# Optimization experiments

Measured on AMD Instinct MI355X. Metric: run time of the kernel, lower is better.

Reference implementation:

```python
import jax, jax.numpy as jnp
import numpy as np

B, N, DIN, D, PHI, RHO, L = 4096, 10, 32, 128, 256, 128, 3
EPS = 1e-5


def setup_inputs() -> dict:
    key = jax.random.key(0)
    ks = jax.random.split(key, 24)
    def p(k, shape):
        return jax.random.normal(k, shape, jnp.float32) * 0.05
    return {
        "A": jax.random.normal(ks[0], (B, N, N), jnp.float32),
        "X": jax.random.normal(ks[1], (B, N, DIN), jnp.float32),
        "home_mask": jax.random.randint(ks[2], (B, N), 0, 2).astype(jnp.int32),
        "We1": p(ks[3], (DIN, D)), "be1": p(ks[4], (D,)),
        "We2": p(ks[5], (D, D)), "be2": p(ks[6], (D,)),
        "rgcn_w": p(ks[7], (L, 2, D, D)),      # per-relation weights
        "rgcn_root": p(ks[8], (L, D, D)),       # root (self) weight
        "rgcn_b": p(ks[9], (L, D)),
        "l1w": p(ks[10], (L, D, D)), "l1b": p(ks[11], (L, D)),
        "l2w": p(ks[12], (L, D, D)), "l2b": p(ks[13], (L, D)),
        "ln_g": jnp.ones((D,), jnp.float32), "ln_b": jnp.zeros((D,), jnp.float32),
        "p1w": p(ks[14], (D, PHI)), "p1b": p(ks[15], (PHI,)),
        "p2w": p(ks[16], (PHI, PHI)), "p2b": p(ks[17], (PHI,)),
        "r1w": p(ks[18], (PHI, RHO)), "r1b": p(ks[19], (RHO,)),
        "r2w": p(ks[20], (RHO, 1)), "r2b": p(ks[21], (1,)),
    }


def _layernorm(x, g, b):
    mu = x.mean(-1, keepdims=True)
    var = ((x - mu) ** 2).mean(-1, keepdims=True)
    return (x - mu) / jnp.sqrt(var + EPS) * g + b


def reference(A, X, home_mask, We1, be1, We2, be2, rgcn_w, rgcn_root, rgcn_b,
              l1w, l1b, l2w, l2b, ln_g, ln_b, p1w, p1b, p2w, p2b,
              r1w, r1b, r2w, r2b):
    BN = B * N
    hm = home_mask.astype(jnp.float32)
    am = 1.0 - hm
    # embedders (dropout layers are identity in eval)
    H = jax.nn.relu(X @ We1 + be1)
    H = (H @ We2 + be2).reshape(BN, D)
    # A ~ randn is nonzero everywhere -> edge list = all (b,i,j) pairs,
    # in the same row-major order torch.nonzero produces.
    bidx = jnp.repeat(jnp.arange(BN), N)          # b*N+i for each edge (row)
    row = bidx
    col = (jnp.repeat(jnp.arange(B), N * N) * N + jnp.tile(jnp.arange(N), BN))
    ew = A.reshape(-1)                             # edge weight
    aw = jnp.abs(ew)
    m1 = (ew > 0).astype(jnp.float32)              # relation 1 mask
    m0 = 1.0 - m1                                  # relation 0 mask
    agg = jnp.zeros_like(H)
    for l in range(L):
        H = H + agg
        # RGCNConv (mean aggregation per relation + root + bias)
        xj = H[row]                                # [E, D] gather of sources
        s0 = jax.ops.segment_sum(xj * m0[:, None], col, num_segments=BN)
        s1 = jax.ops.segment_sum(xj * m1[:, None], col, num_segments=BN)
        c0 = jax.ops.segment_sum(m0, col, num_segments=BN)
        c1 = jax.ops.segment_sum(m1, col, num_segments=BN)
        mean0 = s0 / jnp.maximum(c0, 1.0)[:, None]
        mean1 = s1 / jnp.maximum(c1, 1.0)[:, None]
        H2 = mean0 @ rgcn_w[l, 0] + mean1 @ rgcn_w[l, 1] + H @ rgcn_root[l] + rgcn_b[l]
        # outer gather-scale-scatter
        msg = H2[col] * aw[:, None]                # [E, D]
        agg = jax.ops.segment_sum(msg, row, num_segments=BN)
        agg = jax.nn.relu(_layernorm(agg, ln_g, ln_b))
        # Linear -> ReLU -> (Dropout=id) -> Linear
        agg = jax.nn.relu(agg @ l1w[l] + l1b[l])
        agg = agg @ l2w[l] + l2b[l]
    H = (H + agg).reshape(B, N, D)
    # DeepSet phi (dropout = identity)
    phi = jax.nn.relu(H @ p1w + p1b)
    phi = jax.nn.relu(phi @ p2w + p2b)             # [B, N, PHI]
    hs = (phi * hm[..., None]).sum(axis=1)
    aws = (phi * am[..., None]).sum(axis=1)
    def rho(s):
        return (jax.nn.relu(s @ r1w + r1b) @ r2w + r2b)[..., 0]
    return 0.5 + 0.5 * jnp.tanh(rho(hs) - rho(aws))
```

## Files before the change

### kernel.cpp

```cpp
#include <hip/hip_runtime.h>
#include <math.h>

#define B_    4096
#define N_    10
#define DIN_  32
#define D_    128
#define PHI_  256
#define RHO_  128
#define L_    3
#define EPS_  1e-5f

__device__ __forceinline__ short f2bs(float f) {
    unsigned u = __float_as_uint(f);
    u += 0x7fffu + ((u >> 16) & 1u);
    return (short)(u >> 16);
}
__device__ __forceinline__ float bs2f(short s) {
    return __uint_as_float(((unsigned)(unsigned short)s) << 16);
}

typedef short bf16x8 __attribute__((ext_vector_type(8)));
typedef float f32x4  __attribute__((ext_vector_type(4)));
typedef float v2f    __attribute__((ext_vector_type(2)));

__device__ __forceinline__ v2f splat2(float s) { v2f r; r.x = s; r.y = s; return r; }
__device__ __forceinline__ v2f fma2(v2f a, v2f b, v2f c) { return __builtin_elementwise_fma(a, b, c); }

#define WS_WE1 0
#define WS_WE2 4096
#define WS_RGW 20480
#define WS_RGR 118784
#define WS_L1  167936
#define WS_L2  217088
#define WS_P1  266240
#define WS_P2  299008
#define WS_R1  364544

__global__ __launch_bounds__(64)
void prep_weights(const float* __restrict__ We1, const float* __restrict__ We2,
                  const float* __restrict__ rgw, const float* __restrict__ rgr,
                  const float* __restrict__ l1w, const float* __restrict__ l2w,
                  const float* __restrict__ p1w, const float* __restrict__ p2w,
                  const float* __restrict__ r1w, short* __restrict__ ws)
{
    int bi = blockIdx.x, l = threadIdx.x;
    const float* src; int KS, Nw, dstOff, tt;
    if      (bi <   8) { src = We1; KS = 1; Nw = 128; dstOff = WS_WE1; tt = bi; }
    else if (bi <  40) { src = We2; KS = 4; Nw = 128; dstOff = WS_WE2; tt = bi - 8; }
    else if (bi < 232) { int m = (bi - 40) >> 5;  src = rgw + m * 16384; KS = 4; Nw = 128; dstOff = WS_RGW + m * 16384; tt = (bi - 40)  & 31; }
    else if (bi < 328) { int m = (bi - 232) >> 5; src = rgr + m * 16384; KS = 4; Nw = 128; dstOff = WS_RGR + m * 16384; tt = (bi - 232) & 31; }
    else if (bi < 424) { int m = (bi - 328) >> 5; src = l1w + m * 16384; KS = 4; Nw = 128; dstOff = WS_L1  + m * 16384; tt = (bi - 328) & 31; }
    else if (bi < 520) { int m = (bi - 424) >> 5; src = l2w + m * 16384; KS = 4; Nw = 128; dstOff = WS_L2  + m * 16384; tt = (bi - 424) & 31; }
    else if (bi < 584) { src = p1w; KS = 4; Nw = 256; dstOff = WS_P1; tt = bi - 520; }
    else if (bi < 712) { src = p2w; KS = 8; Nw = 256; dstOff = WS_P2; tt = bi - 584; }
    else               { src = r1w; KS = 8; Nw = 128; dstOff = WS_R1; tt = bi - 712; }
    int nt = tt / KS, ks = tt - nt * KS;
    int kbase = ks * 32 + (l >> 4) * 8;
    int col   = nt * 16 + (l & 15);
    union { short s[8]; int4 v; } u;
#pragma unroll
    for (int j = 0; j < 8; ++j)
        u.s[j] = f2bs(src[(size_t)(kbase + j) * Nw + col]);
    *(int4*)(ws + dstOff + ((size_t)tt * 64 + l) * 8) = u.v;
}


template<int NT>
__device__ __forceinline__ void initC(f32x4* acc, const float* __restrict__ bias, int c16) {
#pragma unroll
    for (int nt = 0; nt < NT; ++nt) {
        float bv = bias[nt * 16 + c16];
        acc[nt] = (f32x4){bv, bv, bv, bv};
    }
}

template<int KS, int NT>
__device__ __forceinline__ void mm_a16(const short* __restrict__ Wf, const short* __restrict__ Ab,
                                       int ldA, int mrow, int q, int l, f32x4* acc) {
#pragma unroll
    for (int ks = 0; ks < KS; ++ks) {
        bf16x8 a = *(const bf16x8*)(Ab + mrow * ldA + ks * 32 + q * 8);
#pragma unroll
        for (int nt = 0; nt < NT; ++nt) {
            bf16x8 bv = *(const bf16x8*)(Wf + ((size_t)(nt * KS + ks) * 64 + l) * 8);
            acc[nt] = __builtin_amdgcn_mfma_f32_16x16x32_bf16(a, bv, acc[nt], 0, 0, 0);
        }
    }
}

template<int KS, int NT>
__device__ __forceinline__ void mm_a32(const short* __restrict__ Wf, const float* __restrict__ Af,
                                       int ldA, int mrow, int q, int l, f32x4* acc) {
#pragma unroll
    for (int ks = 0; ks < KS; ++ks) {
        const float* p = Af + mrow * ldA + ks * 32 + q * 8;
        f32x4 x0 = *(const f32x4*)p;
        f32x4 x1 = *(const f32x4*)(p + 4);
        bf16x8 a;
        a[0] = f2bs(x0[0]); a[1] = f2bs(x0[1]); a[2] = f2bs(x0[2]); a[3] = f2bs(x0[3]);
        a[4] = f2bs(x1[0]); a[5] = f2bs(x1[1]); a[6] = f2bs(x1[2]); a[7] = f2bs(x1[3]);
#pragma unroll
        for (int nt = 0; nt < NT; ++nt) {
            bf16x8 bv = *(const bf16x8*)(Wf + ((size_t)(nt * KS + ks) * 64 + l) * 8);
            acc[nt] = __builtin_amdgcn_mfma_f32_16x16x32_bf16(a, bv, acc[nt], 0, 0, 0);
        }
    }
}

template<int KS>
__device__ __forceinline__ void mm8p_a16(const short* __restrict__ Wf,
                                         const short* __restrict__ Ab, int ldA,
                                         int mrow, int q, int l, f32x4* acc)
{
    const short* ap = Ab + mrow * ldA + q * 8;
    const short* wp = Wf + l * 8;
    bf16x8 acur = *(const bf16x8*)ap;
    bf16x8 bcur[8], bnxt[8];
#pragma unroll
    for (int nt = 0; nt < 8; ++nt) bcur[nt] = *(const bf16x8*)(wp + (size_t)nt * KS * 512);
#pragma unroll
    for (int ks = 0; ks < KS; ++ks) {
        bf16x8 anxt = acur;
#pragma unroll
        for (int nt = 0; nt < 8; ++nt) bnxt[nt] = bcur[nt];
        if (ks + 1 < KS) {
            anxt = *(const bf16x8*)(ap + (ks + 1) * 32);
#pragma unroll
            for (int nt = 0; nt < 8; ++nt)
                bnxt[nt] = *(const bf16x8*)(wp + (size_t)(nt * KS + ks + 1) * 512);
        }
#pragma unroll
        for (int nt = 0; nt < 8; ++nt)
            acc[nt] = __builtin_amdgcn_mfma_f32_16x16x32_bf16(acur, bcur[nt], acc[nt], 0, 0, 0);
        acur = anxt;
#pragma unroll
        for (int nt = 0; nt < 8; ++nt) bcur[nt] = bnxt[nt];
    }
}

template<int KS>
__device__ __forceinline__ void mm8p_a32(const short* __restrict__ Wf,
                                         const float* __restrict__ Af, int ldA,
                                         int mrow, int q, int l, f32x4* acc)
{
    const float* ap = Af + mrow * ldA + q * 8;
    const short* wp = Wf + l * 8;
    auto cvt = [&](int ks) {
        f32x4 x0 = *(const f32x4*)(ap + ks * 32);
        f32x4 x1 = *(const f32x4*)(ap + ks * 32 + 4);
        bf16x8 a;
        a[0] = f2bs(x0[0]); a[1] = f2bs(x0[1]); a[2] = f2bs(x0[2]); a[3] = f2bs(x0[3]);
        a[4] = f2bs(x1[0]); a[5] = f2bs(x1[1]); a[6] = f2bs(x1[2]); a[7] = f2bs(x1[3]);
        return a;
    };
    bf16x8 acur = cvt(0);
    bf16x8 bcur[8], bnxt[8];
#pragma unroll
    for (int nt = 0; nt < 8; ++nt) bcur[nt] = *(const bf16x8*)(wp + (size_t)nt * KS * 512);
#pragma unroll
    for (int ks = 0; ks < KS; ++ks) {
        bf16x8 anxt = acur;
#pragma unroll
        for (int nt = 0; nt < 8; ++nt) bnxt[nt] = bcur[nt];
        if (ks + 1 < KS) {
            anxt = cvt(ks + 1);
#pragma unroll
            for (int nt = 0; nt < 8; ++nt)
                bnxt[nt] = *(const bf16x8*)(wp + (size_t)(nt * KS + ks + 1) * 512);
        }
#pragma unroll
        for (int nt = 0; nt < 8; ++nt)
            acc[nt] = __builtin_amdgcn_mfma_f32_16x16x32_bf16(acur, bcur[nt], acc[nt], 0, 0, 0);
        acur = anxt;
#pragma unroll
        for (int nt = 0; nt < 8; ++nt) bcur[nt] = bnxt[nt];
    }
}

template<int NT, bool RELU>
__device__ __forceinline__ void storeC16(const f32x4* acc, short* __restrict__ dst,
                                         int ldD, int q, int c16) {
#pragma unroll
    for (int nt = 0; nt < NT; ++nt) {
#pragma unroll
        for (int i = 0; i < 4; ++i) {
            int r = q * 4 + i;
            if (r < 10) {
                float v = acc[nt][i];
                if (RELU) v = fmaxf(v, 0.f);
                dst[r * ldD + nt * 16 + c16] = f2bs(v);
            }
        }
    }
}

#define HLD  132
#define GLD  264
#define H2LD 136

__global__ __launch_bounds__(64, 2)
void gcn_main(const float* __restrict__ A, const float* __restrict__ X,
              const int* __restrict__ home_mask,
              const float* __restrict__ be1, const float* __restrict__ be2,
              const float* __restrict__ rgcn_b,
              const float* __restrict__ l1b, const float* __restrict__ l2b,
              const float* __restrict__ ln_g, const float* __restrict__ ln_b,
              const float* __restrict__ p1b, const float* __restrict__ p2b,
              const float* __restrict__ r1b, const float* __restrict__ r2w,
              const short* __restrict__ ws, float* __restrict__ out)
{
    const int b   = blockIdx.x;
    const int l   = threadIdx.x;
    const int q   = l >> 4;
    const int c16 = l & 15;
    const int mrow = (c16 < 10) ? c16 : 9;

    __shared__ __align__(16) float HfS[N_ * HLD];
    __shared__ __align__(16) short GbS[N_ * GLD];
    __shared__ __align__(16) short H2S[N_ * H2LD];
    __shared__ float AabsS[100], M1S[100];
    __shared__ float invc0S[N_], invc1S[N_];
    __shared__ float hmfS[16], awfS[16];

    short* S0 = GbS;
    short* S1 = GbS + 136;
    short* RhoS = H2S;

    {
        const float* Ab = A + (size_t)b * 100;
#pragma unroll
        for (int e = l; e < 100; e += 64) {
            float a = Ab[e];
            AabsS[e] = fabsf(a);
            M1S[e]  = (a > 0.f) ? 1.f : 0.f;
        }
        if (l < 16) {
            float hm = 0.f, aw = 0.f;
            if (l < 10) { hm = (float)home_mask[b * N_ + l]; aw = 1.f - hm; }
            hmfS[l] = hm; awfS[l] = aw;
        }
        if (l < 10) {
            float c1 = 0.f;
#pragma unroll
            for (int i = 0; i < 10; ++i) c1 += M1S[i * 10 + l];
            invc1S[l] = 1.f / fmaxf(c1, 1.f);
            invc0S[l] = 1.f / fmaxf(10.f - c1, 1.f);
        }
    }

    {
        f32x4 acc[8];
        initC<8>(acc, be1, c16);
        const float* xg = X + (size_t)b * (N_ * DIN_) + mrow * DIN_ + q * 8;
        f32x4 x0 = *(const f32x4*)xg;
        f32x4 x1 = *(const f32x4*)(xg + 4);
        bf16x8 a;
        a[0] = f2bs(x0[0]); a[1] = f2bs(x0[1]); a[2] = f2bs(x0[2]); a[3] = f2bs(x0[3]);
        a[4] = f2bs(x1[0]); a[5] = f2bs(x1[1]); a[6] = f2bs(x1[2]); a[7] = f2bs(x1[3]);
#pragma unroll
        for (int nt = 0; nt < 8; ++nt) {
            bf16x8 bv = *(const bf16x8*)(ws + WS_WE1 + ((size_t)nt * 64 + l) * 8);
            acc[nt] = __builtin_amdgcn_mfma_f32_16x16x32_bf16(a, bv, acc[nt], 0, 0, 0);
        }
        storeC16<8, true>(acc, S0, GLD, q, c16);
    }
    {
        f32x4 acc[8];
        initC<8>(acc, be2, c16);
        mm8p_a16<4>(ws + WS_WE2, S0, GLD, mrow, q, l, acc);
#pragma unroll
        for (int nt = 0; nt < 8; ++nt)
#pragma unroll
            for (int i = 0; i < 4; ++i) {
                int r = q * 4 + i;
                if (r < 10) HfS[r * HLD + nt * 16 + c16] = acc[nt][i];
            }
    }

    const v2f lg2 = *(const v2f*)(ln_g + 2 * l);
    const v2f lb2 = *(const v2f*)(ln_b + 2 * l);

    for (int ll = 0; ll < L_; ++ll) {
        {
            v2f hv[N_];
#pragma unroll
            for (int i = 0; i < N_; ++i) hv[i] = *(const v2f*)(HfS + i * HLD + 2 * l);
            v2f st = hv[0];
#pragma unroll
            for (int i = 1; i < N_; ++i) st += hv[i];
#pragma unroll
            for (int j = 0; j < N_; ++j) {
                v2f s1 = splat2(0.f);
#pragma unroll
                for (int i = 0; i < N_; ++i) s1 = fma2(splat2(M1S[i * 10 + j]), hv[i], s1);
                v2f m0 = (st - s1) * splat2(invc0S[j]);
                v2f m1 = s1 * splat2(invc1S[j]);
                short2 w0; w0.x = f2bs(m0.x); w0.y = f2bs(m0.y);
                short2 w1; w1.x = f2bs(m1.x); w1.y = f2bs(m1.y);
                *(short2*)(S0 + j * GLD + 2 * l) = w0;
                *(short2*)(S1 + j * GLD + 2 * l) = w1;
            }
        }
        {
            f32x4 acc[8];
            initC<8>(acc, rgcn_b + ll * D_, c16);
            mm8p_a16<4>(ws + WS_RGW + (size_t)(ll * 2 + 0) * 16384, S0, GLD, mrow, q, l, acc);
            mm8p_a16<4>(ws + WS_RGW + (size_t)(ll * 2 + 1) * 16384, S1, GLD, mrow, q, l, acc);
            mm8p_a32<4>(ws + WS_RGR + (size_t)ll * 16384, HfS, HLD, mrow, q, l, acc);
            storeC16<8, false>(acc, H2S, H2LD, q, c16);
        }
        {
            v2f ag[N_];
#pragma unroll
            for (int i = 0; i < N_; ++i) ag[i] = splat2(0.f);
#pragma unroll
            for (int j = 0; j < N_; ++j) {
                short2 hh = *(const short2*)(H2S + j * H2LD + 2 * l);
                v2f h2; h2.x = bs2f(hh.x); h2.y = bs2f(hh.y);
#pragma unroll
                for (int i = 0; i < N_; ++i)
                    ag[i] = fma2(splat2(AabsS[i * 10 + j]), h2, ag[i]);
            }
#pragma unroll
            for (int i = 0; i < N_; ++i) {
                float s  = ag[i].x + ag[i].y;
                float ss = fmaf(ag[i].x, ag[i].x, ag[i].y * ag[i].y);
#pragma unroll
                for (int off = 32; off > 0; off >>= 1) {
                    s  += __shfl_xor(s,  off);
                    ss += __shfl_xor(ss, off);
                }
                float mu   = s * (1.f / 128.f);
                float var  = ss * (1.f / 128.f) - mu * mu;
                float rstd = rsqrtf(var + EPS_);
                v2f v = fma2((ag[i] - splat2(mu)) * splat2(rstd), lg2, lb2);
                short2 wv; wv.x = f2bs(fmaxf(v.x, 0.f)); wv.y = f2bs(fmaxf(v.y, 0.f));
                *(short2*)(S0 + i * GLD + 2 * l) = wv;
            }
        }
        {
            f32x4 acc[8];
            initC<8>(acc, l1b + ll * D_, c16);
            mm8p_a16<4>(ws + WS_L1 + (size_t)ll * 16384, S0, GLD, mrow, q, l, acc);
            storeC16<8, true>(acc, S1, GLD, q, c16);
        }
        {
            f32x4 acc[8];
            initC<8>(acc, l2b + ll * D_, c16);
            mm8p_a16<4>(ws + WS_L2 + (size_t)ll * 16384, S1, GLD, mrow, q, l, acc);
#pragma unroll
            for (int nt = 0; nt < 8; ++nt)
#pragma unroll
                for (int i = 0; i < 4; ++i) {
                    int r = q * 4 + i;
                    if (r < 10) HfS[r * HLD + nt * 16 + c16] += acc[nt][i];
                }
        }
    }

    {
        f32x4 acc[16];
        initC<16>(acc, p1b, c16);
        mm_a32<4, 16>(ws + WS_P1, HfS, HLD, mrow, q, l, acc);
        storeC16<16, true>(acc, GbS, GLD, q, c16);
    }
    {
        f32x4 acc[16];
        initC<16>(acc, p2b, c16);
        mm_a16<8, 16>(ws + WS_P2, GbS, GLD, mrow, q, l, acc);
        float hm0 = hmfS[q * 4 + 0], hm1 = hmfS[q * 4 + 1], hm2 = hmfS[q * 4 + 2], hm3 = hmfS[q * 4 + 3];
        float aw0 = awfS[q * 4 + 0], aw1 = awfS[q * 4 + 1], aw2 = awfS[q * 4 + 2], aw3 = awfS[q * 4 + 3];
#pragma unroll
        for (int t = 0; t < 16; ++t) {
            float v0 = fmaxf(acc[t][0], 0.f), v1 = fmaxf(acc[t][1], 0.f);
            float v2 = fmaxf(acc[t][2], 0.f), v3 = fmaxf(acc[t][3], 0.f);
            float hp = hm0 * v0 + hm1 * v1 + hm2 * v2 + hm3 * v3;
            float ap = aw0 * v0 + aw1 * v1 + aw2 * v2 + aw3 * v3;
            hp += __shfl_xor(hp, 16); hp += __shfl_xor(hp, 32);
            ap += __shfl_xor(ap, 16); ap += __shfl_xor(ap, 32);
            if (l < 16) {
                RhoS[t * 16 + l]       = f2bs(hp);
                RhoS[256 + t * 16 + l] = f2bs(ap);
            }
        }
    }
    {
        f32x4 acc[8];
        initC<8>(acc, r1b, c16);
        const int rr = (c16 < 2) ? c16 : 0;
        mm_a16<8, 8>(ws + WS_R1, RhoS, 256, rr, q, l, acc);
        float d = 0.f;
        if (q == 0) {
#pragma unroll
            for (int t = 0; t < 8; ++t) {
                float vh = fmaxf(acc[t][0], 0.f);
                float va = fmaxf(acc[t][1], 0.f);
                d = fmaf(vh - va, r2w[t * 16 + c16], d);
            }
        }
#pragma unroll
        for (int off = 32; off > 0; off >>= 1) d += __shfl_xor(d, off);
        if (l == 0) out[b] = 0.5f + 0.5f * tanhf(d);
    }
}

extern "C" void kernel_launch(void* const* d_in, const int* in_sizes, int n_in,
                              void* d_out, int out_size, void* d_ws, size_t ws_size,
                              hipStream_t stream) {
    const float* A         = (const float*)d_in[0];
    const float* X         = (const float*)d_in[1];
    const int*   home_mask = (const int*)  d_in[2];
    const float* We1       = (const float*)d_in[3];
    const float* be1       = (const float*)d_in[4];
    const float* We2       = (const float*)d_in[5];
    const float* be2       = (const float*)d_in[6];
    const float* rgcn_w    = (const float*)d_in[7];
    const float* rgcn_root = (const float*)d_in[8];
    const float* rgcn_b    = (const float*)d_in[9];
    const float* l1w       = (const float*)d_in[10];
    const float* l1b       = (const float*)d_in[11];
    const float* l2w       = (const float*)d_in[12];
    const float* l2b       = (const float*)d_in[13];
    const float* ln_g      = (const float*)d_in[14];
    const float* ln_b      = (const float*)d_in[15];
    const float* p1w       = (const float*)d_in[16];
    const float* p1b       = (const float*)d_in[17];
    const float* p2w       = (const float*)d_in[18];
    const float* p2b       = (const float*)d_in[19];
    const float* r1w       = (const float*)d_in[20];
    const float* r1b       = (const float*)d_in[21];
    const float* r2w       = (const float*)d_in[22];

    short* ws = (short*)d_ws;

    prep_weights<<<776, 64, 0, stream>>>(We1, We2, rgcn_w, rgcn_root,
                                         l1w, l2w, p1w, p2w, r1w, ws);
    gcn_main<<<B_, 64, 0, stream>>>(A, X, home_mask, be1, be2, rgcn_b,
                                    l1b, l2b, ln_g, ln_b, p1b, p2b,
                                    r1b, r2w, ws, (float*)d_out);
}
```

Measured before the change: 253.3 us.

## Pack four graphs per 256-thread block and use packed bf16 conversion

The main kernel now runs four independent graphs per block, one per wavefront, each with its own slice of LDS. Launch bounds change to 256 threads, and the grid shrinks by four. The scalar float-to-bf16 rounding is replaced by the packed two-wide HIP conversion intrinsic. Block-wide __syncthreads calls are added between stages, which are not needed because each wave only touches its own data, so they may add stalls. Larger blocks with quadruple LDS could also change how many waves fit per CU.

```diff
diff --git a/kernel.cpp b/kernel.cpp
--- a/kernel.cpp
+++ b/kernel.cpp
@@ -1,4 +1,5 @@
 #include <hip/hip_runtime.h>
+#include <hip/hip_bf16.h>
 #include <math.h>
 
 #define B_    4096
@@ -17,6 +18,13 @@
 }
 __device__ __forceinline__ float bs2f(short s) {
     return __uint_as_float(((unsigned)(unsigned short)s) << 16);
+}
+__device__ __forceinline__ short2 f2bs2(float x, float y) {
+    float2 f; f.x = x; f.y = y;
+    __hip_bfloat162 h = __float22bfloat162_rn(f);
+    short2 r;
+    __builtin_memcpy(&r, &h, 4);
+    return r;
 }
 
 typedef short bf16x8 __attribute__((ext_vector_type(8)));
@@ -76,13 +84,13 @@
 
 template<int KS, int NT>
 __device__ __forceinline__ void mm_a16(const short* __restrict__ Wf, const short* __restrict__ Ab,
-                                       int ldA, int mrow, int q, int l, f32x4* acc) {
+                                       int ldA, int mrow, int q, int lane, f32x4* acc) {
 #pragma unroll
     for (int ks = 0; ks < KS; ++ks) {
         bf16x8 a = *(const bf16x8*)(Ab + mrow * ldA + ks * 32 + q * 8);
 #pragma unroll
         for (int nt = 0; nt < NT; ++nt) {
-            bf16x8 bv = *(const bf16x8*)(Wf + ((size_t)(nt * KS + ks) * 64 + l) * 8);
+            bf16x8 bv = *(const bf16x8*)(Wf + ((size_t)(nt * KS + ks) * 64 + lane) * 8);
             acc[nt] = __builtin_amdgcn_mfma_f32_16x16x32_bf16(a, bv, acc[nt], 0, 0, 0);
         }
     }
@@ -90,19 +98,19 @@
 
 template<int KS, int NT>
 __device__ __forceinline__ void mm_a32(const short* __restrict__ Wf, const float* __restrict__ Af,
-                                       int ldA, int mrow, int q, int l, f32x4* acc) {
+                                       int ldA, int mrow, int q, int lane, f32x4* acc) {
 #pragma unroll
     for (int ks = 0; ks < KS; ++ks) {
         const float* p = Af + mrow * ldA + ks * 32 + q * 8;
         f32x4 x0 = *(const f32x4*)p;
         f32x4 x1 = *(const f32x4*)(p + 4);
-        bf16x8 a;
-        a[0] = f2bs(x0[0]); a[1] = f2bs(x0[1]); a[2] = f2bs(x0[2]); a[3] = f2bs(x0[3]);
-        a[4] = f2bs(x1[0]); a[5] = f2bs(x1[1]); a[6] = f2bs(x1[2]); a[7] = f2bs(x1[3]);
+        union { short2 p2[4]; bf16x8 v; } a;
+        a.p2[0] = f2bs2(x0[0], x0[1]); a.p2[1] = f2bs2(x0[2], x0[3]);
+        a.p2[2] = f2bs2(x1[0], x1[1]); a.p2[3] = f2bs2(x1[2], x1[3]);
 #pragma unroll
         for (int nt = 0; nt < NT; ++nt) {
-            bf16x8 bv = *(const bf16x8*)(Wf + ((size_t)(nt * KS + ks) * 64 + l) * 8);
-            acc[nt] = __builtin_amdgcn_mfma_f32_16x16x32_bf16(a, bv, acc[nt], 0, 0, 0);
+            bf16x8 bv = *(const bf16x8*)(Wf + ((size_t)(nt * KS + ks) * 64 + lane) * 8);
+            acc[nt] = __builtin_amdgcn_mfma_f32_16x16x32_bf16(a.v, bv, acc[nt], 0, 0, 0);
         }
     }
 }
@@ -110,10 +118,10 @@
 template<int KS>
 __device__ __forceinline__ void mm8p_a16(const short* __restrict__ Wf,
                                          const short* __restrict__ Ab, int ldA,
-                                         int mrow, int q, int l, f32x4* acc)
+                                         int mrow, int q, int lane, f32x4* acc)
 {
     const short* ap = Ab + mrow * ldA + q * 8;
-    const short* wp = Wf + l * 8;
+    const short* wp = Wf + lane * 8;
     bf16x8 acur = *(const bf16x8*)ap;
     bf16x8 bcur[8], bnxt[8];
 #pragma unroll
@@ -141,19 +149,19 @@
 template<int KS>
 __device__ __forceinline__ void mm8p_a32(const short* __restrict__ Wf,
                                          const float* __restrict__ Af, int ldA,
-                                         int mrow, int q, int l, f32x4* acc)
+                                         int mrow, int q, int lane, f32x4* acc)
 {
     const float* ap = Af + mrow * ldA + q * 8;
-    const short* wp = Wf + l * 8;
-    auto cvt = [&](int ks) {
-        f32x4 x0 = *(const f32x4*)(ap + ks * 32);
-        f32x4 x1 = *(const f32x4*)(ap + ks * 32 + 4);
-        bf16x8 a;
-        a[0] = f2bs(x0[0]); a[1] = f2bs(x0[1]); a[2] = f2bs(x0[2]); a[3] = f2bs(x0[3]);
-        a[4] = f2bs(x1[0]); a[5] = f2bs(x1[1]); a[6] = f2bs(x1[2]); a[7] = f2bs(x1[3]);
-        return a;
+    const short* wp = Wf + lane * 8;
+    auto cvt = [](const float* p) {
+        f32x4 x0 = *(const f32x4*)p;
+        f32x4 x1 = *(const f32x4*)(p + 4);
+        union { short2 p2[4]; bf16x8 v; } a;
+        a.p2[0] = f2bs2(x0[0], x0[1]); a.p2[1] = f2bs2(x0[2], x0[3]);
+        a.p2[2] = f2bs2(x1[0], x1[1]); a.p2[3] = f2bs2(x1[2], x1[3]);
+        return a.v;
     };
-    bf16x8 acur = cvt(0);
+    bf16x8 acur = cvt(ap);
     bf16x8 bcur[8], bnxt[8];
 #pragma unroll
     for (int nt = 0; nt < 8; ++nt) bcur[nt] = *(const bf16x8*)(wp + (size_t)nt * KS * 512);
@@ -163,7 +171,7 @@
 #pragma unroll
         for (int nt = 0; nt < 8; ++nt) bnxt[nt] = bcur[nt];
         if (ks + 1 < KS) {
-            anxt = cvt(ks + 1);
+            anxt = cvt(ap + (ks + 1) * 32);
 #pragma unroll
             for (int nt = 0; nt < 8; ++nt)
                 bnxt[nt] = *(const bf16x8*)(wp + (size_t)(nt * KS + ks + 1) * 512);
@@ -198,7 +206,7 @@
 #define GLD  264
 #define H2LD 136
 
-__global__ __launch_bounds__(64, 2)
+__global__ __launch_bounds__(256, 2)
 void gcn_main(const float* __restrict__ A, const float* __restrict__ X,
               const int* __restrict__ home_mask,
               const float* __restrict__ be1, const float* __restrict__ be2,
@@ -209,82 +217,86 @@
               const float* __restrict__ r1b, const float* __restrict__ r2w,
               const short* __restrict__ ws, float* __restrict__ out)
 {
-    const int b   = blockIdx.x;
-    const int l   = threadIdx.x;
-    const int q   = l >> 4;
-    const int c16 = l & 15;
+    const int t    = threadIdx.x;
+    const int w    = t >> 6;
+    const int lane = t & 63;
+    const int q    = lane >> 4;
+    const int c16  = lane & 15;
     const int mrow = (c16 < 10) ? c16 : 9;
-
-    __shared__ __align__(16) float HfS[N_ * HLD];
-    __shared__ __align__(16) short GbS[N_ * GLD];
-    __shared__ __align__(16) short H2S[N_ * H2LD];
-    __shared__ float AabsS[100], M1S[100];
-    __shared__ float invc0S[N_], invc1S[N_];
-    __shared__ float hmfS[16], awfS[16];
-
-    short* S0 = GbS;
-    short* S1 = GbS + 136;
-    short* RhoS = H2S;
+    const int b    = blockIdx.x * 4 + w;
+
+    __shared__ __align__(16) float HfS[4][N_ * HLD];
+    __shared__ __align__(16) short GbS[4][N_ * GLD];
+    __shared__ __align__(16) short H2S[4][N_ * H2LD];
+    __shared__ float AabsS[4][100], M1S[4][100];
+    __shared__ float invc0S[4][N_], invc1S[4][N_];
+    __shared__ float hmfS[4][16], awfS[4][16];
+
+    short* S0   = &GbS[w][0];
+    short* S1   = &GbS[w][136];
+    short* RhoS = &H2S[w][0];
 
     {
         const float* Ab = A + (size_t)b * 100;
 #pragma unroll
-        for (int e = l; e < 100; e += 64) {
+        for (int e = lane; e < 100; e += 64) {
             float a = Ab[e];
-            AabsS[e] = fabsf(a);
-            M1S[e]  = (a > 0.f) ? 1.f : 0.f;
-        }
-        if (l < 16) {
+            AabsS[w][e] = fabsf(a);
+            M1S[w][e]  = (a > 0.f) ? 1.f : 0.f;
+        }
+        if (lane < 16) {
             float hm = 0.f, aw = 0.f;
-            if (l < 10) { hm = (float)home_mask[b * N_ + l]; aw = 1.f - hm; }
-            hmfS[l] = hm; awfS[l] = aw;
-        }
-        if (l < 10) {
+            if (lane < 10) { hm = (float)home_mask[b * N_ + lane]; aw = 1.f - hm; }
+            hmfS[w][lane] = hm; awfS[w][lane] = aw;
+        }
+        if (lane < 10) {
             float c1 = 0.f;
 #pragma unroll
-            for (int i = 0; i < 10; ++i) c1 += M1S[i * 10 + l];
-            invc1S[l] = 1.f / fmaxf(c1, 1.f);
-            invc0S[l] = 1.f / fmaxf(10.f - c1, 1.f);
-        }
-    }
-
+            for (int i = 0; i < 10; ++i) c1 += M1S[w][i * 10 + lane];
+            invc1S[w][lane] = 1.f / fmaxf(c1, 1.f);
+            invc0S[w][lane] = 1.f / fmaxf(10.f - c1, 1.f);
+        }
+    }
+
+    __syncthreads();
     {
         f32x4 acc[8];
         initC<8>(acc, be1, c16);
         const float* xg = X + (size_t)b * (N_ * DIN_) + mrow * DIN_ + q * 8;
         f32x4 x0 = *(const f32x4*)xg;
         f32x4 x1 = *(const f32x4*)(xg + 4);
-        bf16x8 a;
-        a[0] = f2bs(x0[0]); a[1] = f2bs(x0[1]); a[2] = f2bs(x0[2]); a[3] = f2bs(x0[3]);
-        a[4] = f2bs(x1[0]); a[5] = f2bs(x1[1]); a[6] = f2bs(x1[2]); a[7] = f2bs(x1[3]);
+        union { short2 p2[4]; bf16x8 v; } a;
+        a.p2[0] = f2bs2(x0[0], x0[1]); a.p2[1] = f2bs2(x0[2], x0[3]);
+        a.p2[2] = f2bs2(x1[0], x1[1]); a.p2[3] = f2bs2(x1[2], x1[3]);
 #pragma unroll
         for (int nt = 0; nt < 8; ++nt) {
-            bf16x8 bv = *(const bf16x8*)(ws + WS_WE1 + ((size_t)nt * 64 + l) * 8);
-            acc[nt] = __builtin_amdgcn_mfma_f32_16x16x32_bf16(a, bv, acc[nt], 0, 0, 0);
+            bf16x8 bv = *(const bf16x8*)(ws + WS_WE1 + ((size_t)nt * 64 + lane) * 8);
+            acc[nt] = __builtin_amdgcn_mfma_f32_16x16x32_bf16(a.v, bv, acc[nt], 0, 0, 0);
         }
         storeC16<8, true>(acc, S0, GLD, q, c16);
     }
+    __syncthreads();
     {
         f32x4 acc[8];
         initC<8>(acc, be2, c16);
-        mm8p_a16<4>(ws + WS_WE2, S0, GLD, mrow, q, l, acc);
+        mm8p_a16<4>(ws + WS_WE2, S0, GLD, mrow, q, lane, acc);
 #pragma unroll
         for (int nt = 0; nt < 8; ++nt)
 #pragma unroll
             for (int i = 0; i < 4; ++i) {
                 int r = q * 4 + i;
-                if (r < 10) HfS[r * HLD + nt * 16 + c16] = acc[nt][i];
-            }
-    }
-
-    const v2f lg2 = *(const v2f*)(ln_g + 2 * l);
-    const v2f lb2 = *(const v2f*)(ln_b + 2 * l);
+                if (r < 10) HfS[w][r * HLD + nt * 16 + c16] = acc[nt][i];
+            }
+    }
+
+    const v2f lg2 = *(const v2f*)(ln_g + 2 * lane);
+    const v2f lb2 = *(const v2f*)(ln_b + 2 * lane);
 
     for (int ll = 0; ll < L_; ++ll) {
         {
             v2f hv[N_];
 #pragma unroll
-            for (int i = 0; i < N_; ++i) hv[i] = *(const v2f*)(HfS + i * HLD + 2 * l);
+            for (int i = 0; i < N_; ++i) hv[i] = *(const v2f*)(&HfS[w][i * HLD] + 2 * lane);
             v2f st = hv[0];
 #pragma unroll
             for (int i = 1; i < N_; ++i) st += hv[i];
@@ -292,22 +304,21 @@
             for (int j = 0; j < N_; ++j) {
                 v2f s1 = splat2(0.f);
 #pragma unroll
-                for (int i = 0; i < N_; ++i) s1 = fma2(splat2(M1S[i * 10 + j]), hv[i], s1);
-                v2f m0 = (st - s1) * splat2(invc0S[j]);
-                v2f m1 = s1 * splat2(invc1S[j]);
-                short2 w0; w0.x = f2bs(m0.x); w0.y = f2bs(m0.y);
-                short2 w1; w1.x = f2bs(m1.x); w1.y = f2bs(m1.y);
-                *(short2*)(S0 + j * GLD + 2 * l) = w0;
-                *(short2*)(S1 + j * GLD + 2 * l) = w1;
-            }
-        }
+                for (int i = 0; i < N_; ++i) s1 = fma2(splat2(M1S[w][i * 10 + j]), hv[i], s1);
+                v2f m0 = (st - s1) * splat2(invc0S[w][j]);
+                v2f m1 = s1 * splat2(invc1S[w][j]);
+                *(short2*)(S0 + j * GLD + 2 * lane) = f2bs2(m0.x, m0.y);
+                *(short2*)(S1 + j * GLD + 2 * lane) = f2bs2(m1.x, m1.y);
+            }
+        }
+        __syncthreads();
         {
             f32x4 acc[8];
             initC<8>(acc, rgcn_b + ll * D_, c16);
-            mm8p_a16<4>(ws + WS_RGW + (size_t)(ll * 2 + 0) * 16384, S0, GLD, mrow, q, l, acc);
-            mm8p_a16<4>(ws + WS_RGW + (size_t)(ll * 2 + 1) * 16384, S1, GLD, mrow, q, l, acc);
-            mm8p_a32<4>(ws + WS_RGR + (size_t)ll * 16384, HfS, HLD, mrow, q, l, acc);
-            storeC16<8, false>(acc, H2S, H2LD, q, c16);
+            mm8p_a16<4>(ws + WS_RGW + (size_t)(ll * 2 + 0) * 16384, S0, GLD, mrow, q, lane, acc);
+            mm8p_a16<4>(ws + WS_RGW + (size_t)(ll * 2 + 1) * 16384, S1, GLD, mrow, q, lane, acc);
+            mm8p_a32<4>(ws + WS_RGR + (size_t)ll * 16384, &HfS[w][0], HLD, mrow, q, lane, acc);
+            storeC16<8, false>(acc, &H2S[w][0], H2LD, q, c16);
         }
         {
             v2f ag[N_];
@@ -315,11 +326,11 @@
             for (int i = 0; i < N_; ++i) ag[i] = splat2(0.f);
 #pragma unroll
             for (int j = 0; j < N_; ++j) {
-                short2 hh = *(const short2*)(H2S + j * H2LD + 2 * l);
+                short2 hh = *(const short2*)(&H2S[w][j * H2LD] + 2 * lane);
                 v2f h2; h2.x = bs2f(hh.x); h2.y = bs2f(hh.y);
 #pragma unroll
                 for (int i = 0; i < N_; ++i)
-                    ag[i] = fma2(splat2(AabsS[i * 10 + j]), h2, ag[i]);
+                    ag[i] = fma2(splat2(AabsS[w][i * 10 + j]), h2, ag[i]);
             }
 #pragma unroll
             for (int i = 0; i < N_; ++i) {
@@ -334,73 +345,79 @@
                 float var  = ss * (1.f / 128.f) - mu * mu;
                 float rstd = rsqrtf(var + EPS_);
                 v2f v = fma2((ag[i] - splat2(mu)) * splat2(rstd), lg2, lb2);
-                short2 wv; wv.x = f2bs(fmaxf(v.x, 0.f)); wv.y = f2bs(fmaxf(v.y, 0.f));
-                *(short2*)(S0 + i * GLD + 2 * l) = wv;
-            }
-        }
+                *(short2*)(S0 + i * GLD + 2 * lane) = f2bs2(fmaxf(v.x, 0.f), fmaxf(v.y, 0.f));
+            }
+        }
+        __syncthreads();
         {
             f32x4 acc[8];
             initC<8>(acc, l1b + ll * D_, c16);
-            mm8p_a16<4>(ws + WS_L1 + (size_t)ll * 16384, S0, GLD, mrow, q, l, acc);
+            mm8p_a16<4>(ws + WS_L1 + (size_t)ll * 16384, S0, GLD, mrow, q, lane, acc);
             storeC16<8, true>(acc, S1, GLD, q, c16);
         }
+        __syncthreads();
         {
             f32x4 acc[8];
             initC<8>(acc, l2b + ll * D_, c16);
-            mm8p_a16<4>(ws + WS_L2 + (size_t)ll * 16384, S1, GLD, mrow, q, l, acc);
+            mm8p_a16<4>(ws + WS_L2 + (size_t)ll * 16384, S1, GLD, mrow, q, lane, acc);
 #pragma unroll
             for (int nt = 0; nt < 8; ++nt)
 #pragma unroll
                 for (int i = 0; i < 4; ++i) {
                     int r = q * 4 + i;
-                    if (r < 10) HfS[r * HLD + nt * 16 + c16] += acc[nt][i];
+                    if (r < 10) HfS[w][r * HLD + nt * 16 + c16] += acc[nt][i];
                 }
         }
     }
 
+    __syncthreads();
     {
         f32x4 acc[16];
         initC<16>(acc, p1b, c16);
-        mm_a32<4, 16>(ws + WS_P1, HfS, HLD, mrow, q, l, acc);
-        storeC16<16, true>(acc, GbS, GLD, q, c16);
-    }
+        mm_a32<4, 16>(ws + WS_P1, &HfS[w][0], HLD, mrow, q, lane, acc);
+        storeC16<16, true>(acc, &GbS[w][0], GLD, q, c16);
+    }
+    __syncthreads();
     {
         f32x4 acc[16];
         initC<16>(acc, p2b, c16);
-        mm_a16<8, 16>(ws + WS_P2, GbS, GLD, mrow, q, l, acc);
-        float hm0 = hmfS[q * 4 + 0], hm1 = hmfS[q * 4 + 1], hm2 = hmfS[q * 4 + 2], hm3 = hmfS[q * 4 + 3];
-        float aw0 = awfS[q * 4 + 0], aw1 = awfS[q * 4 + 1], aw2 = awfS[q * 4 + 2], aw3 = awfS[q * 4 + 3];
-#pragma unroll
-        for (int t = 0; t < 16; ++t) {
-            float v0 = fmaxf(acc[t][0], 0.f), v1 = fmaxf(acc[t][1], 0.f);
-            float v2 = fmaxf(acc[t][2], 0.f), v3 = fmaxf(acc[t][3], 0.f);
+        mm_a16<8, 16>(ws + WS_P2, &GbS[w][0], GLD, mrow, q, lane, acc);
+        float hm0 = hmfS[w][q * 4 + 0], hm1 = hmfS[w][q * 4 + 1];
+        float hm2 = hmfS[w][q * 4 + 2], hm3 = hmfS[w][q * 4 + 3];
+        float aw0 = awfS[w][q * 4 + 0], aw1 = awfS[w][q * 4 + 1];
+        float aw2 = awfS[w][q * 4 + 2], aw3 = awfS[w][q * 4 + 3];
+#pragma unroll
+        for (int tt = 0; tt < 16; ++tt) {
+            float v0 = fmaxf(acc[tt][0], 0.f), v1 = fmaxf(acc[tt][1], 0.f);
+            float v2 = fmaxf(acc[tt][2], 0.f), v3 = fmaxf(acc[tt][3], 0.f);
             float hp = hm0 * v0 + hm1 * v1 + hm2 * v2 + hm3 * v3;
             float ap = aw0 * v0 + aw1 * v1 + aw2 * v2 + aw3 * v3;
             hp += __shfl_xor(hp, 16); hp += __shfl_xor(hp, 32);
             ap += __shfl_xor(ap, 16); ap += __shfl_xor(ap, 32);
-            if (l < 16) {
-                RhoS[t * 16 + l]       = f2bs(hp);
-                RhoS[256 + t * 16 + l] = f2bs(ap);
-            }
-        }
-    }
+            if (lane < 16) {
+                RhoS[tt * 16 + lane]       = f2bs(hp);
+                RhoS[256 + tt * 16 + lane] = f2bs(ap);
+            }
+        }
+    }
+    __syncthreads();
     {
         f32x4 acc[8];
         initC<8>(acc, r1b, c16);
         const int rr = (c16 < 2) ? c16 : 0;
-        mm_a16<8, 8>(ws + WS_R1, RhoS, 256, rr, q, l, acc);
+        mm_a16<8, 8>(ws + WS_R1, RhoS, 256, rr, q, lane, acc);
         float d = 0.f;
         if (q == 0) {
 #pragma unroll
-            for (int t = 0; t < 8; ++t) {
-                float vh = fmaxf(acc[t][0], 0.f);
-                float va = fmaxf(acc[t][1], 0.f);
-                d = fmaf(vh - va, r2w[t * 16 + c16], d);
+            for (int tt = 0; tt < 8; ++tt) {
+                float vh = fmaxf(acc[tt][0], 0.f);
+                float va = fmaxf(acc[tt][1], 0.f);
+                d = fmaf(vh - va, r2w[tt * 16 + c16], d);
             }
         }
 #pragma unroll
         for (int off = 32; off > 0; off >>= 1) d += __shfl_xor(d, off);
-        if (l == 0) out[b] = 0.5f + 0.5f * tanhf(d);
+        if (lane == 0) out[b] = 0.5f + 0.5f * tanhf(d);
     }
 }
 
@@ -435,7 +452,7 @@
 
     prep_weights<<<776, 64, 0, stream>>>(We1, We2, rgcn_w, rgcn_root,
                                          l1w, l2w, p1w, p2w, r1w, ws);
-    gcn_main<<<B_, 64, 0, stream>>>(A, X, home_mask, be1, be2, rgcn_b,
-                                    l1b, l2b, ln_g, ln_b, p1b, p2b,
-                                    r1b, r2w, ws, (float*)d_out);
-}
+    gcn_main<<<B_ / 4, 256, 0, stream>>>(A, X, home_mask, be1, be2, rgcn_b,
+                                         l1b, l2b, ln_g, ln_b, p1b, p2b,
+                                         r1b, r2w, ws, (float*)d_out);
+}
```

Measured after the change: 260.9 us. +3.0%, slower.
